# Optimization experiments

Measured on AMD Instinct MI355X. Metric: run time of the kernel, lower is better.

Reference implementation:

```python
import jax, jax.numpy as jnp
import numpy as np

NUM_ITERATIONS = 3
EPS = 1e-8


def _squash_elementwise(t):
    # Faithful to the torch code: squared_norm sums over dim=-1 which has
    # size 1 in s_j (B,1,C,O,1), so squash acts per-element.
    sq = t * t
    return sq / (1.0 + sq) * t / jnp.sqrt(sq + EPS)


def setup_inputs() -> dict:
    key = jax.random.key(0)
    kx, kw = jax.random.split(key)
    batch, in_ch, num_routes = 128, 64, 1152
    num_caps, out_ch = 16, 64
    x = jax.random.normal(kx, (batch, in_ch, num_routes), dtype=jnp.float32)
    # W ~ torch.randn(1, num_routes, num_capsules, out_channels, in_channels)
    W = jax.random.normal(kw, (1, num_routes, num_caps, out_ch, in_ch), dtype=jnp.float32)
    return {"x": x, "W": W}


def reference(x, W):
    # x: (B, in_ch, R) -> (B, R, in_ch)
    xt = jnp.swapaxes(x, 1, 2)
    # u_hat[b,r,c,o] = sum_i W[0,r,c,o,i] * x[b,r,i]
    u_hat = jnp.einsum('rcoi,bri->brco', W[0], xt)  # (B, R, C, O)
    B, R, C, O = u_hat.shape
    b_ij = jnp.zeros((B, R, C), dtype=u_hat.dtype)
    v = None
    for it in range(NUM_ITERATIONS):
        c_ij = jax.nn.softmax(b_ij, axis=2)                 # (B, R, C)
        s_j = jnp.einsum('brc,brco->bco', c_ij, u_hat)      # (B, C, O)
        v = _squash_elementwise(s_j)                        # (B, C, O)
        if it < NUM_ITERATIONS - 1:
            a_ij = jnp.einsum('brco,bco->brc', u_hat, v)    # agreement
            b_ij = b_ij + a_ij
    # torch returns v_j.squeeze(1) of shape (B, C, O, 1)
    return v[..., None]
```

## Files before the change

### kernel.cpp

```cpp
#include <hip/hip_runtime.h>
#include <hip/hip_bf16.h>

#define R_ 1152
#define B_ 128
#define I_ 64
#define C_ 16
#define O_ 64
#define CO_ 1024

typedef float f32x16 __attribute__((ext_vector_type(16)));

__global__ __launch_bounds__(512, 1) void uhat_kernel(const float* __restrict__ x,
                                                      const float* __restrict__ W,
                                                      float* __restrict__ u) {
  const int r = blockIdx.x;
  const int t = threadIdx.x;
  __shared__ float xl[I_][B_ + 4];

  const float4* wp = (const float4*)(W + ((size_t)r * CO_ + 2 * t) * I_);
  float4 wa[16], wb[16];
#pragma unroll
  for (int q = 0; q < 16; ++q) wa[q] = wp[q];
#pragma unroll
  for (int q = 0; q < 16; ++q) wb[q] = wp[16 + q];

#pragma unroll
  for (int k = 0; k < 16; ++k) {
    int bi = t + k * 512;
    xl[bi & 63][bi >> 6] = x[(size_t)bi * R_ + r];
  }
  __syncthreads();

  const size_t bstride = (size_t)R_ * CO_;
  const size_t obase = (size_t)r * CO_ + 2 * t;
#pragma unroll 1
  for (int b0 = 0; b0 < B_; b0 += 4) {
    float2 acc[4];
#pragma unroll
    for (int j = 0; j < 4; ++j) { acc[j].x = 0.f; acc[j].y = 0.f; }
#pragma unroll
    for (int q = 0; q < 16; ++q) {
      float4 xv0 = *(const float4*)&xl[4 * q + 0][b0];
      float4 xv1 = *(const float4*)&xl[4 * q + 1][b0];
      float4 xv2 = *(const float4*)&xl[4 * q + 2][b0];
      float4 xv3 = *(const float4*)&xl[4 * q + 3][b0];
#define STEP(xv, wc0, wc1)                                   \
      acc[0].x += xv.x * (wc0); acc[0].y += xv.x * (wc1);    \
      acc[1].x += xv.y * (wc0); acc[1].y += xv.y * (wc1);    \
      acc[2].x += xv.z * (wc0); acc[2].y += xv.z * (wc1);    \
      acc[3].x += xv.w * (wc0); acc[3].y += xv.w * (wc1);
      STEP(xv0, wa[q].x, wb[q].x)
      STEP(xv1, wa[q].y, wb[q].y)
      STEP(xv2, wa[q].z, wb[q].z)
      STEP(xv3, wa[q].w, wb[q].w)
#undef STEP
    }
#pragma unroll
    for (int j = 0; j < 4; ++j) {
      *(float2*)&u[obase + (size_t)(b0 + j) * bstride] = acc[j];
    }
  }
}

template <int MODE>
__global__ __launch_bounds__(256) void route_kernel(const float* __restrict__ u,
                                                    const float* __restrict__ vprev,
                                                    float* __restrict__ bij,
                                                    float* __restrict__ s) {
  const int blk = blockIdx.x;
  const int b = blk / 36;
  const int rc = blk % 36;
  const int w = threadIdx.x >> 6;
  const int l = threadIdx.x & 63;

  f32x16 vv;
  if (MODE != 0) {
    vv = *(const f32x16*)(vprev + (size_t)b * CO_ + l * 16);
  }
  f32x16 sacc;
#pragma unroll
  for (int j = 0; j < 16; ++j) sacc[j] = 0.f;

  for (int k = 0; k < 8; ++k) {
    const int r = rc * 32 + w * 8 + k;
    const f32x16 uu = *(const f32x16*)(u + ((size_t)b * R_ + r) * CO_ + l * 16);
    float cval;
    if (MODE == 0) {
      cval = 1.0f / 16.0f;
    } else {
      float p = 0.f;
#pragma unroll
      for (int j = 0; j < 16; ++j) p += uu[j] * vv[j];
      p += __shfl_xor(p, 1);
      p += __shfl_xor(p, 2);
      float bn = p;
      const size_t bidx = ((size_t)b * R_ + r) * C_ + (l >> 2);
      if (MODE == 2) bn += bij[bidx];
      if (MODE == 1 && (l & 3) == 0) bij[bidx] = bn;
      float mx = bn;
#pragma unroll
      for (int d = 1; d < 64; d <<= 1) mx = fmaxf(mx, __shfl_xor(mx, d));
      float e = __expf(bn - mx);
      float tot = e;
#pragma unroll
      for (int d = 1; d < 64; d <<= 1) tot += __shfl_xor(tot, d);
      cval = 4.0f * e / tot;
    }
#pragma unroll
    for (int j = 0; j < 16; ++j) sacc[j] += cval * uu[j];
  }

  __shared__ float sp[4][16][64];
#pragma unroll
  for (int j = 0; j < 16; ++j) sp[w][j][l] = sacc[j];
  __syncthreads();
#pragma unroll
  for (int q = 0; q < 4; ++q) {
    const int co = threadIdx.x + q * 256;
    const int jj = co & 15, ll = co >> 4;
    float val = sp[0][jj][ll] + sp[1][jj][ll] + sp[2][jj][ll] + sp[3][jj][ll];
    atomicAdd(&s[(size_t)b * CO_ + co], val);
  }
}

__global__ __launch_bounds__(256) void squash_kernel(const float* __restrict__ s,
                                                     float* __restrict__ v) {
  const int i = blockIdx.x * 256 + threadIdx.x;
  const float t = s[i];
  const float sq = t * t;
  v[i] = sq / (1.0f + sq) * t * rsqrtf(sq + 1e-8f);
}

extern "C" void kernel_launch(void* const* d_in, const int* in_sizes, int n_in,
                              void* d_out, int out_size, void* d_ws, size_t ws_size,
                              hipStream_t stream) {
  (void)in_sizes; (void)n_in; (void)out_size; (void)ws_size;
  const float* x = (const float*)d_in[0];
  const float* W = (const float*)d_in[1];
  float* out = (float*)d_out;

  char* ws = (char*)d_ws;
  float* u = (float*)ws;
  size_t off = (size_t)B_ * R_ * CO_ * sizeof(float);
  float* bij = (float*)(ws + off);
  off += (size_t)B_ * R_ * C_ * sizeof(float);
  float* s = (float*)(ws + off);
  off += (size_t)B_ * CO_ * sizeof(float);
  float* vbuf = (float*)(ws + off);

  const size_t s_bytes = (size_t)B_ * CO_ * sizeof(float);

  uhat_kernel<<<R_, 512, 0, stream>>>(x, W, u);

  hipMemsetAsync(s, 0, s_bytes, stream);
  route_kernel<0><<<B_ * 36, 256, 0, stream>>>(u, nullptr, bij, s);
  squash_kernel<<<(B_ * CO_) / 256, 256, 0, stream>>>(s, vbuf);

  hipMemsetAsync(s, 0, s_bytes, stream);
  route_kernel<1><<<B_ * 36, 256, 0, stream>>>(u, vbuf, bij, s);
  squash_kernel<<<(B_ * CO_) / 256, 256, 0, stream>>>(s, vbuf);

  hipMemsetAsync(s, 0, s_bytes, stream);
  route_kernel<2><<<B_ * 36, 256, 0, stream>>>(u, vbuf, bij, s);
  squash_kernel<<<(B_ * CO_) / 256, 256, 0, stream>>>(s, out);
}
```

Measured before the change: 1.159 ms.

## Permute u_hat layout for coalesced routing loads and split uhat blocks per route

The u_hat output is written in a permuted order inside each route row, so the routing kernel can read it with four coalesced float4 loads per lane instead of one 64-byte vector per lane. uhat_kernel now uses two blocks per route, each handling 512 outputs with one weight row per thread, and a swizzled block order; the x transpose load is reorganised. The routing kernel also prefetches the b_ij values before its loop in the last iteration. The trade-off is that x is reloaded into shared memory twice per route, and the implicit layout contract between the two kernels becomes harder to follow.

```diff
diff --git a/kernel.cpp b/kernel.cpp
--- a/kernel.cpp
+++ b/kernel.cpp
@@ -10,55 +10,57 @@
 
 typedef float f32x16 __attribute__((ext_vector_type(16)));
 
-__global__ __launch_bounds__(512, 1) void uhat_kernel(const float* __restrict__ x,
-                                                      const float* __restrict__ W,
-                                                      float* __restrict__ u) {
-  const int r = blockIdx.x;
+
+__global__ __launch_bounds__(512) void uhat_kernel(const float* __restrict__ x,
+                                                   const float* __restrict__ W,
+                                                   float* __restrict__ u) {
+  const int id = blockIdx.x;
+  const int swz = (id & 7) * 288 + (id >> 3);
+  const int r = swz >> 1;
+  const int h = swz & 1;
   const int t = threadIdx.x;
+
   __shared__ float xl[I_][B_ + 4];
+#pragma unroll
+  for (int p = 0; p < 16; ++p) {
+    const int b = t & 127;
+    const int i = (t >> 7) + p * 4;
+    xl[i][b] = x[((size_t)(b * 64 + i)) * R_ + r];
+  }
 
-  const float4* wp = (const float4*)(W + ((size_t)r * CO_ + 2 * t) * I_);
-  float4 wa[16], wb[16];
+  const int plin = h * 512 + t;
+  const int l = (plin >> 2) & 63;
+  const int j4 = plin >> 8;
+  const int e = plin & 3;
+  const int co = l * 16 + j4 * 4 + e;
+
+  float4 w[16];
+  const float4* wp = (const float4*)(W + ((size_t)r * CO_ + co) * I_);
 #pragma unroll
-  for (int q = 0; q < 16; ++q) wa[q] = wp[q];
-#pragma unroll
-  for (int q = 0; q < 16; ++q) wb[q] = wp[16 + q];
+  for (int q = 0; q < 16; ++q) w[q] = wp[q];
 
-#pragma unroll
-  for (int k = 0; k < 16; ++k) {
-    int bi = t + k * 512;
-    xl[bi & 63][bi >> 6] = x[(size_t)bi * R_ + r];
-  }
   __syncthreads();
 
+  float* uout = u + (size_t)r * CO_ + plin;
   const size_t bstride = (size_t)R_ * CO_;
-  const size_t obase = (size_t)r * CO_ + 2 * t;
 #pragma unroll 1
   for (int b0 = 0; b0 < B_; b0 += 4) {
-    float2 acc[4];
-#pragma unroll
-    for (int j = 0; j < 4; ++j) { acc[j].x = 0.f; acc[j].y = 0.f; }
+    float acc0 = 0.f, acc1 = 0.f, acc2 = 0.f, acc3 = 0.f;
 #pragma unroll
     for (int q = 0; q < 16; ++q) {
-      float4 xv0 = *(const float4*)&xl[4 * q + 0][b0];
-      float4 xv1 = *(const float4*)&xl[4 * q + 1][b0];
-      float4 xv2 = *(const float4*)&xl[4 * q + 2][b0];
-      float4 xv3 = *(const float4*)&xl[4 * q + 3][b0];
-#define STEP(xv, wc0, wc1)                                   \
-      acc[0].x += xv.x * (wc0); acc[0].y += xv.x * (wc1);    \
-      acc[1].x += xv.y * (wc0); acc[1].y += xv.y * (wc1);    \
-      acc[2].x += xv.z * (wc0); acc[2].y += xv.z * (wc1);    \
-      acc[3].x += xv.w * (wc0); acc[3].y += xv.w * (wc1);
-      STEP(xv0, wa[q].x, wb[q].x)
-      STEP(xv1, wa[q].y, wb[q].y)
-      STEP(xv2, wa[q].z, wb[q].z)
-      STEP(xv3, wa[q].w, wb[q].w)
-#undef STEP
+      const float4 xv0 = *(const float4*)&xl[4 * q + 0][b0];
+      const float4 xv1 = *(const float4*)&xl[4 * q + 1][b0];
+      const float4 xv2 = *(const float4*)&xl[4 * q + 2][b0];
+      const float4 xv3 = *(const float4*)&xl[4 * q + 3][b0];
+      acc0 += w[q].x * xv0.x; acc0 += w[q].y * xv1.x; acc0 += w[q].z * xv2.x; acc0 += w[q].w * xv3.x;
+      acc1 += w[q].x * xv0.y; acc1 += w[q].y * xv1.y; acc1 += w[q].z * xv2.y; acc1 += w[q].w * xv3.y;
+      acc2 += w[q].x * xv0.z; acc2 += w[q].y * xv1.z; acc2 += w[q].z * xv2.z; acc2 += w[q].w * xv3.z;
+      acc3 += w[q].x * xv0.w; acc3 += w[q].y * xv1.w; acc3 += w[q].z * xv2.w; acc3 += w[q].w * xv3.w;
     }
-#pragma unroll
-    for (int j = 0; j < 4; ++j) {
-      *(float2*)&u[obase + (size_t)(b0 + j) * bstride] = acc[j];
-    }
+    uout[(size_t)(b0 + 0) * bstride] = acc0;
+    uout[(size_t)(b0 + 1) * bstride] = acc1;
+    uout[(size_t)(b0 + 2) * bstride] = acc2;
+    uout[(size_t)(b0 + 3) * bstride] = acc3;
   }
 }
 
@@ -72,42 +74,60 @@
   const int rc = blk % 36;
   const int w = threadIdx.x >> 6;
   const int l = threadIdx.x & 63;
+  const int rbase = rc * 32 + w * 8;
 
   f32x16 vv;
   if (MODE != 0) {
     vv = *(const f32x16*)(vprev + (size_t)b * CO_ + l * 16);
   }
-  f32x16 sacc;
+
+  float bpre[8];
+  if (MODE == 2) {
+#pragma unroll
+    for (int k = 0; k < 8; ++k)
+      bpre[k] = bij[((size_t)b * R_ + rbase + k) * C_ + (l >> 2)];
+  }
+
+  float sacc[16];
 #pragma unroll
   for (int j = 0; j < 16; ++j) sacc[j] = 0.f;
 
+  const float* ub0 = u + ((size_t)b * R_ + rbase) * CO_ + l * 4;
+#pragma unroll
   for (int k = 0; k < 8; ++k) {
-    const int r = rc * 32 + w * 8 + k;
-    const f32x16 uu = *(const f32x16*)(u + ((size_t)b * R_ + r) * CO_ + l * 16);
+    const float* ub = ub0 + (size_t)k * CO_;
+    const float4 u0 = *(const float4*)(ub + 0);
+    const float4 u1 = *(const float4*)(ub + 256);
+    const float4 u2 = *(const float4*)(ub + 512);
+    const float4 u3 = *(const float4*)(ub + 768);
     float cval;
     if (MODE == 0) {
       cval = 1.0f / 16.0f;
     } else {
       float p = 0.f;
-#pragma unroll
-      for (int j = 0; j < 16; ++j) p += uu[j] * vv[j];
+      p += u0.x * vv[0];  p += u0.y * vv[1];  p += u0.z * vv[2];  p += u0.w * vv[3];
+      p += u1.x * vv[4];  p += u1.y * vv[5];  p += u1.z * vv[6];  p += u1.w * vv[7];
+      p += u2.x * vv[8];  p += u2.y * vv[9];  p += u2.z * vv[10]; p += u2.w * vv[11];
+      p += u3.x * vv[12]; p += u3.y * vv[13]; p += u3.z * vv[14]; p += u3.w * vv[15];
       p += __shfl_xor(p, 1);
       p += __shfl_xor(p, 2);
       float bn = p;
-      const size_t bidx = ((size_t)b * R_ + r) * C_ + (l >> 2);
-      if (MODE == 2) bn += bij[bidx];
-      if (MODE == 1 && (l & 3) == 0) bij[bidx] = bn;
+      if (MODE == 2) bn += bpre[k];
+      if (MODE == 1 && (l & 3) == 0)
+        bij[((size_t)b * R_ + rbase + k) * C_ + (l >> 2)] = bn;
       float mx = bn;
 #pragma unroll
       for (int d = 1; d < 64; d <<= 1) mx = fmaxf(mx, __shfl_xor(mx, d));
-      float e = __expf(bn - mx);
-      float tot = e;
+      float ex = __expf(bn - mx);
+      float tot = ex;
 #pragma unroll
       for (int d = 1; d < 64; d <<= 1) tot += __shfl_xor(tot, d);
-      cval = 4.0f * e / tot;
+      cval = 4.0f * ex / tot;
     }
-#pragma unroll
-    for (int j = 0; j < 16; ++j) sacc[j] += cval * uu[j];
+    sacc[0]  += cval * u0.x; sacc[1]  += cval * u0.y; sacc[2]  += cval * u0.z; sacc[3]  += cval * u0.w;
+    sacc[4]  += cval * u1.x; sacc[5]  += cval * u1.y; sacc[6]  += cval * u1.z; sacc[7]  += cval * u1.w;
+    sacc[8]  += cval * u2.x; sacc[9]  += cval * u2.y; sacc[10] += cval * u2.z; sacc[11] += cval * u2.w;
+    sacc[12] += cval * u3.x; sacc[13] += cval * u3.y; sacc[14] += cval * u3.z; sacc[15] += cval * u3.w;
   }
 
   __shared__ float sp[4][16][64];
@@ -150,7 +170,7 @@
 
   const size_t s_bytes = (size_t)B_ * CO_ * sizeof(float);
 
-  uhat_kernel<<<R_, 512, 0, stream>>>(x, W, u);
+  uhat_kernel<<<2 * R_, 512, 0, stream>>>(x, W, u);
 
   hipMemsetAsync(s, 0, s_bytes, stream);
   route_kernel<0><<<B_ * 36, 256, 0, stream>>>(u, nullptr, bij, s);
```

Result: faster. 1.067 ms (-7.9%).
